# Kernel optimization log

Measured on AMD Instinct MI355X. Metric: run time of the kernel, lower is better.

Reference implementation:

```python
import jax, jax.numpy as jnp
import numpy as np

N_NODES = 100000
N_EDGES = 3200000
F_IN = 128
HIDDEN = 16
OUT_DIM = 16
NUM_GRAPHS = 64


def setup_inputs() -> dict:
    key = jax.random.key(0)
    ks = jax.random.split(key, 9)
    x = jax.random.normal(ks[0], (N_NODES, F_IN), dtype=jnp.float32)
    edge_index = jax.random.randint(ks[1], (2, N_EDGES), 0, N_NODES, dtype=jnp.int32)
    batch = jnp.sort(jax.random.randint(ks[2], (N_NODES,), 0, NUM_GRAPHS, dtype=jnp.int32))
    W1 = jax.random.normal(ks[3], (F_IN, HIDDEN), dtype=jnp.float32) * (1.0 / np.sqrt(F_IN))
    b1 = jnp.zeros((HIDDEN,), dtype=jnp.float32)
    W2 = jax.random.normal(ks[4], (HIDDEN, OUT_DIM), dtype=jnp.float32) * (1.0 / np.sqrt(HIDDEN))
    b2 = jnp.zeros((OUT_DIM,), dtype=jnp.float32)
    fc_w = jax.random.normal(ks[5], (OUT_DIM, 1), dtype=jnp.float32) * (1.0 / np.sqrt(OUT_DIM))
    fc_b = jnp.zeros((1,), dtype=jnp.float32)
    return {"x": x, "edge_index": edge_index, "batch": batch,
            "W1": W1, "b1": b1, "W2": W2, "b2": b2, "fc_w": fc_w, "fc_b": fc_b}


def _gcn_conv(x, edge_index, W, b):
    """PyG GCNConv: x' = D^-1/2 (A+I) D^-1/2 (x W) + b (with self-loops)."""
    n = x.shape[0]
    h = x @ W  # transform first (small dim), then propagate
    src, dst = edge_index[0], edge_index[1]
    # degree including the self-loop (+1)
    deg = jax.ops.segment_sum(jnp.ones(src.shape, h.dtype), dst, num_segments=n) + 1.0
    dis = jax.lax.rsqrt(deg)  # deg >= 1 so no zeros
    norm = dis[src] * dis[dst]  # [E]
    agg = jax.ops.segment_sum(h[src] * norm[:, None], dst, num_segments=n)
    # self-loop contribution: norm_ii = dis[i]^2
    return agg + (dis * dis)[:, None] * h + b


def reference(x, edge_index, batch, W1, b1, W2, b2, fc_w, fc_b):
    h = jax.nn.relu(_gcn_conv(x, edge_index, W1, b1))
    # F.dropout(training=False) in eval mode is identity
    h = jax.nn.relu(_gcn_conv(h, edge_index, W2, b2))
    pooled = jax.ops.segment_sum(h, batch, num_segments=NUM_GRAPHS)  # global_add_pool
    return jax.nn.sigmoid(pooled @ fc_w + fc_b)  # [NUM_GRAPHS, 1]
```

## Files before the change

### kernel.cpp

```cpp
#include <hip/hip_runtime.h>
#include <hip/hip_fp16.h>
#include <math.h>

#define N_NODES 100000
#define N_EDGES 3200000
#define F_IN    128
#define NGRAPH  64

#define NB      256
#define BWIDTH  391
#define BIN_CAP 15000
#define EPB     4096

typedef int   iv4 __attribute__((ext_vector_type(4)));
typedef float fv4 __attribute__((ext_vector_type(4)));
typedef float fv2 __attribute__((ext_vector_type(2)));

#define OFF_BINCUR 0
#define OFF_DIS    512
#define OFF_ROWR   100864
#define OFF_COL    301056
#define OFF_BINNED 3501056
#define OFF_HINH   3501056
#define OFF_BUFB   4301824

__global__ void __launch_bounds__(512)
bin_k(const int* __restrict__ ei, int* __restrict__ binCursor,
      int* __restrict__ binned) {
    __shared__ int cntL[NB], cnt2[NB], gbase[NB];
    int tid = threadIdx.x;
    if (tid < NB) { cntL[tid] = 0; cnt2[tid] = 0; }
    __syncthreads();
    int myBase = blockIdx.x * EPB + tid * 8;
    bool act = (myBase < N_EDGES);
    int s[8], d[8];
    if (act) {
        const iv4* sp = (const iv4*)(ei + myBase);
        const iv4* dp = (const iv4*)(ei + N_EDGES + myBase);
        iv4 a = __builtin_nontemporal_load(sp);
        iv4 b2 = __builtin_nontemporal_load(sp + 1);
        iv4 c = __builtin_nontemporal_load(dp);
        iv4 e = __builtin_nontemporal_load(dp + 1);
        s[0]=a.x; s[1]=a.y; s[2]=a.z; s[3]=a.w; s[4]=b2.x; s[5]=b2.y; s[6]=b2.z; s[7]=b2.w;
        d[0]=c.x; d[1]=c.y; d[2]=c.z; d[3]=c.w; d[4]=e.x; d[5]=e.y; d[6]=e.z; d[7]=e.w;
#pragma unroll
        for (int k = 0; k < 8; ++k)
            atomicAdd(&cntL[(unsigned)d[k] / BWIDTH], 1);
    }
    __syncthreads();
    if (tid < NB) gbase[tid] = atomicAdd(&binCursor[tid], cntL[tid]);
    __syncthreads();
    if (act) {
#pragma unroll
        for (int k = 0; k < 8; ++k) {
            int b = (unsigned)d[k] / BWIDTH;
            int off = atomicAdd(&cnt2[b], 1);
            binned[(size_t)b * BIN_CAP + gbase[b] + off] = ((d[k] - b * BWIDTH) << 17) | s[k];
        }
    }
}

__global__ void __launch_bounds__(512)
sort_k(const int* __restrict__ binCursor, const int* __restrict__ binned,
       float* __restrict__ dis, int2* __restrict__ rowRange, int* __restrict__ col) {
    __shared__ int cnt[BWIDTH];
    __shared__ int rowLoc[BWIDTH + 1];
    __shared__ int cur[BWIDTH];
    __shared__ int wsum[8];
    __shared__ int ebs;
    int b = blockIdx.x, tid = threadIdx.x;
    if (tid < 256) cnt[tid] = (tid < b) ? binCursor[tid] : 0;
    __syncthreads();
#pragma unroll
    for (int st = 128; st > 0; st >>= 1) {
        if (tid < st) cnt[tid] += cnt[tid + st];
        __syncthreads();
    }
    if (tid == 0) ebs = cnt[0];
    __syncthreads();
    for (int k = tid; k < BWIDTH; k += 512) cnt[k] = 0;
    __syncthreads();
    int n = binCursor[b];
    const int* bb = binned + (size_t)b * BIN_CAP;
    for (int i = tid; i < n; i += 512)
        atomicAdd(&cnt[bb[i] >> 17], 1);
    __syncthreads();
    int base = b * BWIDTH;
    int bw = min(BWIDTH, N_NODES - base);
    for (int k = tid; k < bw; k += 512)
        dis[base + k] = rsqrtf((float)cnt[k] + 1.0f);
    int a = (tid < BWIDTH) ? cnt[tid] : 0;
    int lane = tid & 63, wid = tid >> 6;
    int sc = a;
#pragma unroll
    for (int d = 1; d < 64; d <<= 1) {
        int o = __shfl_up(sc, d);
        if (lane >= d) sc += o;
    }
    if (lane == 63) wsum[wid] = sc;
    __syncthreads();
    int woff = 0;
    for (int w = 0; w < wid; ++w) woff += wsum[w];
    if (tid < BWIDTH) {
        int excl = woff + sc - a;
        rowLoc[tid] = excl;
        cur[tid] = excl;
    }
    if (tid == 0) rowLoc[BWIDTH] = n;
    __syncthreads();
    int eb = ebs;
    for (int k = tid; k < bw; k += 512) {
        int2 rr; rr.x = eb + rowLoc[k]; rr.y = eb + rowLoc[k + 1];
        rowRange[base + k] = rr;
    }
    for (int i = tid; i < n; i += 512) {
        int p = bb[i];
        int pos = atomicAdd(&cur[p >> 17], 1);
        col[eb + pos] = p & 0x1FFFF;
    }
}

__global__ void transform1_k(const float* __restrict__ x, const float* __restrict__ W,
                             const float* __restrict__ dis, __half* __restrict__ outh) {
    int i = blockIdx.x * blockDim.x + threadIdx.x;
    if (i >= N_NODES) return;
    const fv4* xr = (const fv4*)(x + (size_t)i * F_IN);
    float acc[16];
#pragma unroll
    for (int j = 0; j < 16; ++j) acc[j] = 0.f;
#pragma unroll 4
    for (int k4 = 0; k4 < F_IN / 4; ++k4) {
        fv4 xv = xr[k4];
#pragma unroll
        for (int kk = 0; kk < 4; ++kk) {
            int k = k4 * 4 + kk;
            float xk = xv[kk];
#pragma unroll
            for (int j = 0; j < 16; ++j)
                acc[j] = fmaf(xk, W[k * 16 + j], acc[j]);
        }
    }
    float di = dis[i];
    __half2 t[8];
#pragma unroll
    for (int q = 0; q < 8; ++q)
        t[q] = __floats2half2_rn(di * acc[2 * q], di * acc[2 * q + 1]);
    iv4* o = (iv4*)(outh + (size_t)i * 16);
    o[0] = *(iv4*)&t[0];
    o[1] = *(iv4*)&t[4];
}

__global__ void transform2_k(const float* __restrict__ h, const float* __restrict__ W,
                             const float* __restrict__ dis, __half* __restrict__ outh) {
    int i = blockIdx.x * blockDim.x + threadIdx.x;
    if (i >= N_NODES) return;
    const fv4* hr = (const fv4*)(h + (size_t)i * 16);
    float hv[16];
#pragma unroll
    for (int q = 0; q < 4; ++q) {
        fv4 t = hr[q];
        hv[q * 4 + 0] = t.x; hv[q * 4 + 1] = t.y; hv[q * 4 + 2] = t.z; hv[q * 4 + 3] = t.w;
    }
    float acc[16];
#pragma unroll
    for (int j = 0; j < 16; ++j) acc[j] = 0.f;
#pragma unroll
    for (int k = 0; k < 16; ++k) {
#pragma unroll
        for (int j = 0; j < 16; ++j)
            acc[j] = fmaf(hv[k], W[k * 16 + j], acc[j]);
    }
    float di = dis[i];
    __half2 t[8];
#pragma unroll
    for (int q = 0; q < 8; ++q)
        t[q] = __floats2half2_rn(di * acc[2 * q], di * acc[2 * q + 1]);
    iv4* o = (iv4*)(outh + (size_t)i * 16);
    o[0] = *(iv4*)&t[0];
    o[1] = *(iv4*)&t[4];
}

__global__ void prop_k(const __half* __restrict__ hinh, const float* __restrict__ dis,
                       const int2* __restrict__ rowRange, const int* __restrict__ col,
                       const float* __restrict__ bias, float* __restrict__ hout) {
    int gid = blockIdx.x * blockDim.x + threadIdx.x;
    int node = gid >> 3;
    int j = gid & 7;
    if (node >= N_NODES) return;
    int2 rr = rowRange[node];
    const __half2* hh = (const __half2*)hinh;
    float ax0 = 0.f, ay0 = 0.f, ax1 = 0.f, ay1 = 0.f;
    float ax2 = 0.f, ay2 = 0.f, ax3 = 0.f, ay3 = 0.f;
    int e = rr.x;
    for (; e + 4 <= rr.y; e += 4) {
        int s0 = col[e];
        int s1 = col[e + 1];
        int s2 = col[e + 2];
        int s3 = col[e + 3];
        float2 f0 = __half22float2(hh[s0 * 8 + j]);
        float2 f1 = __half22float2(hh[s1 * 8 + j]);
        float2 f2 = __half22float2(hh[s2 * 8 + j]);
        float2 f3 = __half22float2(hh[s3 * 8 + j]);
        ax0 += f0.x; ay0 += f0.y;
        ax1 += f1.x; ay1 += f1.y;
        ax2 += f2.x; ay2 += f2.y;
        ax3 += f3.x; ay3 += f3.y;
    }
    for (; e < rr.y; ++e) {
        float2 f = __half22float2(hh[col[e] * 8 + j]);
        ax0 += f.x; ay0 += f.y;
    }
    float2 self = __half22float2(hh[node * 8 + j]);
    float di = dis[node];
    fv2 bj = ((const fv2*)bias)[j];
    float sx = (ax0 + ax1) + (ax2 + ax3) + self.x;
    float sy = (ay0 + ay1) + (ay2 + ay3) + self.y;
    fv2 v;
    v.x = fmaxf(fmaf(di, sx, bj.x), 0.f);
    v.y = fmaxf(fmaf(di, sy, bj.y), 0.f);
    ((fv2*)hout)[node * 8 + j] = v;
}

__global__ void pool_k(const float* __restrict__ h2, const int* __restrict__ batch,
                       const float* __restrict__ fcw, const float* __restrict__ fcb,
                       float* __restrict__ out) {
    __shared__ float partial[16][16];
    int g = blockIdx.x;
    int lane16 = threadIdx.x & 15, grp = threadIdx.x >> 4;
    int lo = 0, hi = N_NODES;
    while (lo < hi) { int m = (lo + hi) >> 1; if (batch[m] < g) lo = m + 1; else hi = m; }
    int start = lo;
    lo = start; hi = N_NODES;
    while (lo < hi) { int m = (lo + hi) >> 1; if (batch[m] < g + 1) lo = m + 1; else hi = m; }
    int end = lo;
    float acc = 0.f;
    for (int i = start + grp; i < end; i += 16) acc += h2[i * 16 + lane16];
    partial[grp][lane16] = acc;
    __syncthreads();
    if (threadIdx.x < 16) {
        float s = 0.f;
#pragma unroll
        for (int gg = 0; gg < 16; ++gg) s += partial[gg][threadIdx.x];
        partial[0][threadIdx.x] = s * fcw[threadIdx.x];
    }
    __syncthreads();
    if (threadIdx.x == 0) {
        float z = fcb[0];
#pragma unroll
        for (int j = 0; j < 16; ++j) z += partial[0][j];
        out[g] = 1.0f / (1.0f + expf(-z));
    }
}

extern "C" void kernel_launch(void* const* d_in, const int* in_sizes, int n_in,
                              void* d_out, int out_size, void* d_ws, size_t ws_size,
                              hipStream_t stream) {
    const float* x    = (const float*)d_in[0];
    const int*   ei   = (const int*)d_in[1];
    const int*   batch= (const int*)d_in[2];
    const float* W1   = (const float*)d_in[3];
    const float* b1   = (const float*)d_in[4];
    const float* W2   = (const float*)d_in[5];
    const float* b2   = (const float*)d_in[6];
    const float* fcw  = (const float*)d_in[7];
    const float* fcb  = (const float*)d_in[8];
    float* out = (float*)d_out;

    float* ws = (float*)d_ws;
    int*    binCur   = (int*)(ws + OFF_BINCUR);
    float*  dis      = ws + OFF_DIS;
    int2*   rowRange = (int2*)(ws + OFF_ROWR);
    int*    col      = (int*)(ws + OFF_COL);
    int*    binned   = (int*)(ws + OFF_BINNED);
    __half* hinH     = (__half*)(ws + OFF_HINH);
    float*  bufB     = ws + OFF_BUFB;

    (void)hipMemsetAsync(binCur, 0, NB * sizeof(int), stream);

    const int B = 256;
    int gN   = (N_NODES + B - 1) / B;
    int gNP  = (N_NODES * 8 + B - 1) / B;
    int gBin = (N_EDGES + EPB - 1) / EPB;

    bin_k<<<gBin, 512, 0, stream>>>(ei, binCur, binned);
    sort_k<<<NB, 512, 0, stream>>>(binCur, binned, dis, rowRange, col);

    transform1_k<<<gN, B, 0, stream>>>(x, W1, dis, hinH);
    prop_k<<<gNP, B, 0, stream>>>(hinH, dis, rowRange, col, b1, bufB);
    transform2_k<<<gN, B, 0, stream>>>(bufB, W2, dis, hinH);
    prop_k<<<gNP, B, 0, stream>>>(hinH, dis, rowRange, col, b2, bufB);
    pool_k<<<NGRAPH, B, 0, stream>>>(bufB, batch, fcw, fcb, out);
}
```

Before: 176.5 us.

## Use 512 bins for edge sort and 2 threads per node in propagation

Doubles the number of destination bins (smaller bin width) so sort_k launches 512 blocks, each handling fewer nodes, which spreads the CSR build across more CUs. The propagation kernel now assigns two threads per node, each loading 16-byte vectors of eight half features per neighbor instead of eight threads each loading a half2. This cuts the redundant col[] index loads per node and issues wider gathers, at the cost of fewer threads in flight and more registers per thread. Workspace offsets are recomputed for the padded node count.

```diff
diff --git a/kernel.cpp b/kernel.cpp
--- a/kernel.cpp
+++ b/kernel.cpp
@@ -7,29 +7,35 @@
 #define F_IN    128
 #define NGRAPH  64
 
-#define NB      256
-#define BWIDTH  391
-#define BIN_CAP 15000
+#define NB      512
+#define BWIDTH  196
+#define NPAD    100352
+#define BIN_CAP 7200
 #define EPB     4096
 
 typedef int   iv4 __attribute__((ext_vector_type(4)));
 typedef float fv4 __attribute__((ext_vector_type(4)));
 typedef float fv2 __attribute__((ext_vector_type(2)));
 
+__device__ __forceinline__ float2 h2u(int u) {
+    __half2 h = *(__half2*)&u;
+    return __half22float2(h);
+}
+
 #define OFF_BINCUR 0
 #define OFF_DIS    512
-#define OFF_ROWR   100864
-#define OFF_COL    301056
-#define OFF_BINNED 3501056
-#define OFF_HINH   3501056
-#define OFF_BUFB   4301824
+#define OFF_ROWR   (512 + NPAD)
+#define OFF_COL    (512 + NPAD * 3)
+#define OFF_BINNED (OFF_COL + N_EDGES)
+#define OFF_HINH   OFF_BINNED
+#define OFF_BUFB   (OFF_BINNED + NPAD * 8)
 
 __global__ void __launch_bounds__(512)
 bin_k(const int* __restrict__ ei, int* __restrict__ binCursor,
       int* __restrict__ binned) {
     __shared__ int cntL[NB], cnt2[NB], gbase[NB];
     int tid = threadIdx.x;
-    if (tid < NB) { cntL[tid] = 0; cnt2[tid] = 0; }
+    cntL[tid] = 0; cnt2[tid] = 0;
     __syncthreads();
     int myBase = blockIdx.x * EPB + tid * 8;
     bool act = (myBase < N_EDGES);
@@ -48,7 +54,7 @@
             atomicAdd(&cntL[(unsigned)d[k] / BWIDTH], 1);
     }
     __syncthreads();
-    if (tid < NB) gbase[tid] = atomicAdd(&binCursor[tid], cntL[tid]);
+    gbase[tid] = atomicAdd(&binCursor[tid], cntL[tid]);
     __syncthreads();
     if (act) {
 #pragma unroll
@@ -63,22 +69,22 @@
 __global__ void __launch_bounds__(512)
 sort_k(const int* __restrict__ binCursor, const int* __restrict__ binned,
        float* __restrict__ dis, int2* __restrict__ rowRange, int* __restrict__ col) {
+    __shared__ int red[NB];
     __shared__ int cnt[BWIDTH];
     __shared__ int rowLoc[BWIDTH + 1];
     __shared__ int cur[BWIDTH];
     __shared__ int wsum[8];
     __shared__ int ebs;
     int b = blockIdx.x, tid = threadIdx.x;
-    if (tid < 256) cnt[tid] = (tid < b) ? binCursor[tid] : 0;
-    __syncthreads();
-#pragma unroll
-    for (int st = 128; st > 0; st >>= 1) {
-        if (tid < st) cnt[tid] += cnt[tid + st];
+    red[tid] = (tid < b) ? binCursor[tid] : 0;
+    __syncthreads();
+#pragma unroll
+    for (int st = 256; st > 0; st >>= 1) {
+        if (tid < st) red[tid] += red[tid + st];
         __syncthreads();
     }
-    if (tid == 0) ebs = cnt[0];
-    __syncthreads();
-    for (int k = tid; k < BWIDTH; k += 512) cnt[k] = 0;
+    if (tid == 0) ebs = red[0];
+    if (tid < BWIDTH) cnt[tid] = 0;
     __syncthreads();
     int n = binCursor[b];
     const int* bb = binned + (size_t)b * BIN_CAP;
@@ -87,8 +93,8 @@
     __syncthreads();
     int base = b * BWIDTH;
     int bw = min(BWIDTH, N_NODES - base);
-    for (int k = tid; k < bw; k += 512)
-        dis[base + k] = rsqrtf((float)cnt[k] + 1.0f);
+    if (tid < bw)
+        dis[base + tid] = rsqrtf((float)cnt[tid] + 1.0f);
     int a = (tid < BWIDTH) ? cnt[tid] : 0;
     int lane = tid & 63, wid = tid >> 6;
     int sc = a;
@@ -109,9 +115,9 @@
     if (tid == 0) rowLoc[BWIDTH] = n;
     __syncthreads();
     int eb = ebs;
-    for (int k = tid; k < bw; k += 512) {
-        int2 rr; rr.x = eb + rowLoc[k]; rr.y = eb + rowLoc[k + 1];
-        rowRange[base + k] = rr;
+    if (tid < bw) {
+        int2 rr; rr.x = eb + rowLoc[tid]; rr.y = eb + rowLoc[tid + 1];
+        rowRange[base + tid] = rr;
     }
     for (int i = tid; i < n; i += 512) {
         int p = bb[i];
@@ -184,41 +190,60 @@
                        const int2* __restrict__ rowRange, const int* __restrict__ col,
                        const float* __restrict__ bias, float* __restrict__ hout) {
     int gid = blockIdx.x * blockDim.x + threadIdx.x;
-    int node = gid >> 3;
-    int j = gid & 7;
+    int node = gid >> 1;
+    int j = gid & 1;
     if (node >= N_NODES) return;
     int2 rr = rowRange[node];
-    const __half2* hh = (const __half2*)hinh;
-    float ax0 = 0.f, ay0 = 0.f, ax1 = 0.f, ay1 = 0.f;
-    float ax2 = 0.f, ay2 = 0.f, ax3 = 0.f, ay3 = 0.f;
+    const iv4* hh = (const iv4*)hinh;
+    float acc[8];
+#pragma unroll
+    for (int q = 0; q < 8; ++q) acc[q] = 0.f;
     int e = rr.x;
     for (; e + 4 <= rr.y; e += 4) {
         int s0 = col[e];
         int s1 = col[e + 1];
         int s2 = col[e + 2];
         int s3 = col[e + 3];
-        float2 f0 = __half22float2(hh[s0 * 8 + j]);
-        float2 f1 = __half22float2(hh[s1 * 8 + j]);
-        float2 f2 = __half22float2(hh[s2 * 8 + j]);
-        float2 f3 = __half22float2(hh[s3 * 8 + j]);
-        ax0 += f0.x; ay0 += f0.y;
-        ax1 += f1.x; ay1 += f1.y;
-        ax2 += f2.x; ay2 += f2.y;
-        ax3 += f3.x; ay3 += f3.y;
+        iv4 r0 = hh[s0 * 2 + j];
+        iv4 r1 = hh[s1 * 2 + j];
+        iv4 r2 = hh[s2 * 2 + j];
+        iv4 r3 = hh[s3 * 2 + j];
+#pragma unroll
+        for (int q = 0; q < 4; ++q) {
+            float2 f0 = h2u(r0[q]);
+            float2 f1 = h2u(r1[q]);
+            float2 f2 = h2u(r2[q]);
+            float2 f3 = h2u(r3[q]);
+            acc[2 * q]     += (f0.x + f1.x) + (f2.x + f3.x);
+            acc[2 * q + 1] += (f0.y + f1.y) + (f2.y + f3.y);
+        }
     }
     for (; e < rr.y; ++e) {
-        float2 f = __half22float2(hh[col[e] * 8 + j]);
-        ax0 += f.x; ay0 += f.y;
-    }
-    float2 self = __half22float2(hh[node * 8 + j]);
+        iv4 r = hh[col[e] * 2 + j];
+#pragma unroll
+        for (int q = 0; q < 4; ++q) {
+            float2 f = h2u(r[q]);
+            acc[2 * q]     += f.x;
+            acc[2 * q + 1] += f.y;
+        }
+    }
+    iv4 rs = hh[node * 2 + j];
     float di = dis[node];
-    fv2 bj = ((const fv2*)bias)[j];
-    float sx = (ax0 + ax1) + (ax2 + ax3) + self.x;
-    float sy = (ay0 + ay1) + (ay2 + ay3) + self.y;
-    fv2 v;
-    v.x = fmaxf(fmaf(di, sx, bj.x), 0.f);
-    v.y = fmaxf(fmaf(di, sy, bj.y), 0.f);
-    ((fv2*)hout)[node * 8 + j] = v;
+    const fv4* bp = (const fv4*)bias;
+    fv4 b0 = bp[2 * j], b1 = bp[2 * j + 1];
+    float bs[8] = { b0.x, b0.y, b0.z, b0.w, b1.x, b1.y, b1.z, b1.w };
+    float vout[8];
+#pragma unroll
+    for (int q = 0; q < 4; ++q) {
+        float2 f = h2u(rs[q]);
+        vout[2 * q]     = fmaxf(fmaf(di, acc[2 * q] + f.x, bs[2 * q]), 0.f);
+        vout[2 * q + 1] = fmaxf(fmaf(di, acc[2 * q + 1] + f.y, bs[2 * q + 1]), 0.f);
+    }
+    fv4* o = (fv4*)(hout + (size_t)node * 16 + j * 8);
+    fv4 o0 = { vout[0], vout[1], vout[2], vout[3] };
+    fv4 o1 = { vout[4], vout[5], vout[6], vout[7] };
+    o[0] = o0;
+    o[1] = o1;
 }
 
 __global__ void pool_k(const float* __restrict__ h2, const int* __restrict__ batch,
@@ -279,7 +304,7 @@
 
     const int B = 256;
     int gN   = (N_NODES + B - 1) / B;
-    int gNP  = (N_NODES * 8 + B - 1) / B;
+    int gNP  = (N_NODES * 2 + B - 1) / B;
     int gBin = (N_EDGES + EPB - 1) / EPB;
 
     bin_k<<<gBin, 512, 0, stream>>>(ei, binCur, binned);
```

Measured after the change: 184.9 us. +4.7%, slower.
